# Performance work log

Hardware: AMD Instinct MI355X
Metric: run time of the kernel (lower is better)

The kernel has to match this reference:

```python
import jax, jax.numpy as jnp
import numpy as np
from jax.scipy.special import logsumexp

K = 15          # top-k
N = 4096        # n candidates
BS = 128        # batch size
EPS = 0.1       # entropic regularizer epsilon
MAX_ITER = 200  # Sinkhorn iterations
RANK = 5        # rank of pseudoinverse init
SMALL = 1e-20


def _build_weights():
    """Rank-5 pseudoinverse of Sinkhorn constraint matrix A (as in __init__).
    A maps (f in R^n, g in R^k) -> (f_i + g_c) over rows r = i*(k+1)+c (g_k := 0).
    A^T A = [[(k+1) I_n, J_{n x k}], [J_{k x n}, n I_k]] in closed form."""
    k1 = K + 1
    p = N + K
    G = np.zeros((p, p), dtype=np.float64)
    G[:N, :N] = (k1) * np.eye(N)
    G[:N, N:] = 1.0
    G[N:, :N] = 1.0
    G[N:, N:] = N * np.eye(K)
    w, V = np.linalg.eigh(G)
    idx = np.argsort(w)[-RANK:]
    s = np.sqrt(w[idx])
    V = V[:, idx]                                  # (p, RANK)
    # U = A @ V / s without materializing A (1GB dense):
    vf = V[:N]                                     # (N, RANK)
    vg = np.concatenate([V[N:], np.zeros((1, RANK))], axis=0)  # (k1, RANK)
    U = (vf[:, None, :] + vg[None, :, :]).reshape(N * k1, RANK) / s
    weight1 = (V / s).astype(np.float32)           # (N+K, RANK) = V diag(1/s)
    weight2 = U.T.astype(np.float32)               # (RANK, N*(K+1)) = U^T
    return jnp.asarray(weight1), jnp.asarray(weight2)


def setup_inputs() -> dict:
    key = jax.random.key(0)
    scores = jax.random.normal(key, (BS, N), dtype=jnp.float32)
    tau = jnp.ones((1,), jnp.float32) * 0.1
    weight1, weight2 = _build_weights()
    return {"scores": scores, "tau": tau, "weight1": weight1, "weight2": weight2}


def _sinkhorn(C, mu, nu, Gamma0, weight1, weight2):
    bs, n, k1 = C.shape
    # least-squares warm start for potentials f, g
    b = (C + EPS * jnp.log(Gamma0)).reshape(bs, -1)          # (bs, n*k1)
    x = jnp.einsum('bm,rm->br', b, weight2)                  # (bs, RANK)
    x = jnp.einsum('br,pr->bp', x, weight1)                  # (bs, n+k)
    f = x[:, :n, None]                                       # (bs, n, 1)
    g = jnp.concatenate([x[:, n:], jnp.zeros((bs, 1), C.dtype)], axis=-1)[:, None, :]  # (bs,1,k1)
    elog_mu = EPS * jnp.log(mu)                              # (1, n, 1)
    elog_nu = EPS * jnp.log(nu)                              # (1, 1, k1)

    def step(carry, _):
        f, g = carry
        f = -EPS * logsumexp(-(C - g) / EPS, axis=-1, keepdims=True) + elog_mu
        g = -EPS * logsumexp(-(C - f) / EPS, axis=-2, keepdims=True) + elog_nu
        return (f, g), None

    (f, g), _ = jax.lax.scan(step, (f, g), None, length=MAX_ITER)
    return jnp.exp((-C + f + g) / EPS)


def reference(scores, tau, weight1, weight2):
    bs, n = scores.shape
    k = K
    s = scores[:, :, None]                                   # (bs, n, 1)
    sd = jax.lax.stop_gradient(s)
    max_s = jnp.max(sd)
    min_s = jnp.min(jnp.where(jnp.isneginf(sd), jnp.inf, sd))
    filled = min_s - (max_s - min_s)
    s = jnp.where(jnp.isneginf(s), filled, s)
    anchors = jnp.arange(k, -1, -1, dtype=s.dtype).reshape(1, 1, k + 1)
    C = (s - anchors) ** 2
    C = C / jax.lax.stop_gradient(C.max())
    mu = jnp.full((1, n, 1), 1.0 / n, dtype=s.dtype)
    nu = jnp.concatenate([jnp.full((k,), 1.0 / n), jnp.array([(n - k) / n])]).astype(s.dtype).reshape(1, 1, k + 1)
    # warm-start transport plan Gamma0 from (detached) hard top-k
    topk_val = jax.lax.top_k(jax.lax.stop_gradient(s[..., 0]), k)[0]      # (bs, k)
    Gamma0 = jax.nn.sigmoid(-jnp.abs(topk_val[:, None, :] - s) / tau)     # (bs, n, k)
    Gamma0 = Gamma0 + SMALL
    Gamma0 = Gamma0 / Gamma0.sum(-2, keepdims=True) / n
    Gamma0_last = jnp.clip(1.0 / n - Gamma0.sum(-1, keepdims=True), SMALL, 1.0 - SMALL)
    Gamma0 = jnp.concatenate([Gamma0, Gamma0_last], axis=-1)              # (bs, n, k+1)
    Gamma = _sinkhorn(C, mu, nu, Gamma0, weight1, weight2)
    A = Gamma[:, :, :k] * n
    return A, jnp.linalg.norm(Gamma - Gamma0)
```

## Files before the change

kernel.cpp:

```cpp
#include <hip/hip_runtime.h>
#include <math.h>

#define KK 15
#define K1 16
#define NN 4096
#define BSZ 128
#define NT 512
#define RPT 8
#define NPAIR 4
#define NW 8
#define EPSI 0.1f
#define SMALLC 1e-20f
#define NITER 200
#define W2STRIDE 65536
#define OUT_A_ELEMS (BSZ * NN * KK)
#define TS 20
#define CONV_REL 5e-7f

typedef __attribute__((ext_vector_type(2))) float f2;
typedef __attribute__((ext_vector_type(2))) unsigned u2v;
__device__ __forceinline__ f2 pk_fma(f2 a, f2 b, f2 c){
  return __builtin_elementwise_fma(a, b, c);
}

__device__ __forceinline__ unsigned enc_f32(float f){
  unsigned u = __float_as_uint(f);
  return (u & 0x80000000u) ? ~u : (u | 0x80000000u);
}
__device__ __forceinline__ float dec_f32(unsigned e){
  unsigned u = (e & 0x80000000u) ? (e ^ 0x80000000u) : ~e;
  return __uint_as_float(u);
}


template<int CTRL>
__device__ __forceinline__ float dpp_movf(float x){
  return __uint_as_float((unsigned)__builtin_amdgcn_update_dpp(
      (int)0, (int)__float_as_uint(x), CTRL, 0xF, 0xF, true));
}

__device__ __forceinline__ float xsum16(float r){
#if __has_builtin(__builtin_amdgcn_permlane16_swap)
  u2v s = __builtin_amdgcn_permlane16_swap(__float_as_uint(r), __float_as_uint(r), false, false);
  return __uint_as_float(s.x) + __uint_as_float(s.y);
#else
  return r + __shfl_xor(r, 16);
#endif
}
__device__ __forceinline__ float xsum32(float r){
#if __has_builtin(__builtin_amdgcn_permlane32_swap)
  u2v s = __builtin_amdgcn_permlane32_swap(__float_as_uint(r), __float_as_uint(r), false, false);
  return __uint_as_float(s.x) + __uint_as_float(s.y);
#else
  return r + __shfl_xor(r, 32);
#endif
}

__device__ __forceinline__ int fold_col(int lane){
  int l = lane & 15;
  return ((l & 1) << 3) | ((l & 2) << 1) | ((l & 8) >> 2) | ((l & 4) >> 2);
}

__device__ __forceinline__ float wave_fold16(const float p[K1], int lane){
  float a[8];
  {
    const bool hi = (lane & 1) != 0;
    #pragma unroll
    for (int j = 0; j < 8; ++j){
      float send = hi ? p[j] : p[j + 8];
      float keep = hi ? p[j + 8] : p[j];
      a[j] = keep + dpp_movf<0xB1>(send);
    }
  }
  float bq[4];
  {
    const bool hi = (lane & 2) != 0;
    #pragma unroll
    for (int j = 0; j < 4; ++j){
      float send = hi ? a[j] : a[j + 4];
      float keep = hi ? a[j + 4] : a[j];
      bq[j] = keep + dpp_movf<0x4E>(send);
    }
  }
  float cq[2];
  {
    const bool hi = (lane & 8) != 0;
    float s0 = hi ? bq[0] : bq[2];
    float s1 = hi ? bq[1] : bq[3];
    float k0 = hi ? bq[2] : bq[0];
    float k1 = hi ? bq[3] : bq[1];
    cq[0] = k0 + dpp_movf<0x128>(s0);
    cq[1] = k1 + dpp_movf<0x128>(s1);
  }
  float r;
  {
    const bool hi = (lane & 4) != 0;
    float send = hi ? cq[0] : cq[1];
    float keep = hi ? cq[1] : cq[0];
    r = keep + __shfl_xor(send, 4);
  }
  r = xsum16(r);
  r = xsum32(r);
  return r;
}

__device__ __forceinline__ void block_fold16(const float p[K1], float* wb, float* tb,
                                             int lane, int wv, int tid){
  float r = wave_fold16(p, lane);
  if (lane < 16) wb[wv * K1 + fold_col(lane)] = r;
  __syncthreads();
  if (tid < 16){
    float t = 0.0f;
    #pragma unroll
    for (int q = 0; q < NW; ++q) t += wb[q * K1 + tid];
    tb[tid] = t;
  }
  __syncthreads();
}

__global__ __launch_bounds__(NT, 2) void k_main(
    const float* __restrict__ scores, const float* __restrict__ taup,
    const float* __restrict__ w1, const float* __restrict__ w2,
    float* __restrict__ out, unsigned* __restrict__ ws){
  const int b = blockIdx.x;
  const int tid = threadIdx.x;
  const int lane = tid & 63;
  const int wv = tid >> 6;

  __shared__ float scratch[NN];
  __shared__ float tk[KK];
  __shared__ int tki[KK];
  __shared__ __align__(16) float cbuf[K1];
  __shared__ float wbuf[NW * K1];
  __shared__ __align__(16) float xbuf[K1];
  __shared__ __align__(16) float wbufT[2][K1 * TS];
  __shared__ float rv[NW];
  __shared__ int ri[NW];
  __shared__ float rmn[NW];
  __shared__ unsigned sng[NW];
  __shared__ float statb[4];

  float raw[RPT];
  #pragma unroll
  for (int j = 0; j < RPT; ++j) raw[j] = scores[(size_t)b * NN + tid + NT * j];

  {
    float mx = -INFINITY, mn = INFINITY; unsigned neg = 0u;
    #pragma unroll
    for (int j = 0; j < RPT; ++j){
      float v = raw[j];
      mx = fmaxf(mx, v);
      if (v == -INFINITY) neg = 1u; else mn = fminf(mn, v);
    }
    #pragma unroll
    for (int off = 32; off; off >>= 1){
      mx = fmaxf(mx, __shfl_xor(mx, off));
      mn = fminf(mn, __shfl_xor(mn, off));
      neg |= (unsigned)__shfl_xor((int)neg, off);
    }
    if (lane == 0){ rv[wv] = mx; rmn[wv] = mn; sng[wv] = neg; }
    __syncthreads();
    if (tid == 0){
      for (int q = 1; q < NW; ++q){
        mx = fmaxf(mx, rv[q]); mn = fminf(mn, rmn[q]); neg |= sng[q];
      }
      atomicMax(&ws[0], enc_f32(mx));
      atomicMin(&ws[5], enc_f32(mn));
      if (neg) atomicOr(&ws[1], 1u);
      __threadfence();
      atomicAdd(&ws[3], 1u);
      while (__hip_atomic_load(&ws[3], __ATOMIC_ACQUIRE, __HIP_MEMORY_SCOPE_AGENT) < (unsigned)BSZ)
        __builtin_amdgcn_s_sleep(2);
      statb[0] = dec_f32(__hip_atomic_load(&ws[0], __ATOMIC_RELAXED, __HIP_MEMORY_SCOPE_AGENT));
      statb[1] = dec_f32(__hip_atomic_load(&ws[5], __ATOMIC_RELAXED, __HIP_MEMORY_SCOPE_AGENT));
      statb[2] = __hip_atomic_load(&ws[1], __ATOMIC_RELAXED, __HIP_MEMORY_SCOPE_AGENT) ? 1.0f : 0.0f;
    }
    __syncthreads();
  }

  const float smax = statb[0];
  const float smin_raw = statb[1];
  const bool has_neg = statb[2] != 0.0f;
  const float filled = smin_raw - (smax - smin_raw);
  const float smin_eff = has_neg ? filled : smin_raw;
  const float cmax = fmaxf(fmaxf(smin_eff * smin_eff, smax * smax),
                           fmaxf((smin_eff - 15.0f) * (smin_eff - 15.0f),
                                 (smax - 15.0f) * (smax - 15.0f)));
  const float cinv = 1.0f / cmax;
  const float tauv = taup[0];
  const float invtau = 1.0f / tauv;
  const float inv_n = 1.0f / (float)NN;

  #pragma unroll
  for (int j = 0; j < RPT; ++j){
    float v = raw[j]; if (v == -INFINITY) v = filled;
    scratch[tid + NT * j] = v;
  }
  __syncthreads();

  for (int t = 0; t < KK; ++t){
    float bv = -INFINITY; int bi = NN;
    #pragma unroll
    for (int j = 0; j < RPT; ++j){
      int i = tid + NT * j;
      float v = scratch[i];
      if (v > bv){ bv = v; bi = i; }
    }
    #pragma unroll
    for (int off = 32; off; off >>= 1){
      float ov = __shfl_xor(bv, off);
      int oi = __shfl_xor(bi, off);
      if (ov > bv || (ov == bv && oi < bi)){ bv = ov; bi = oi; }
    }
    if (lane == 0){ rv[wv] = bv; ri[wv] = bi; }
    __syncthreads();
    if (tid == 0){
      for (int q = 1; q < NW; ++q){
        if (rv[q] > bv || (rv[q] == bv && ri[q] < bi)){ bv = rv[q]; bi = ri[q]; }
      }
      tk[t] = bv;
      tki[t] = bi;
      scratch[bi] = -INFINITY;
    }
    __syncthreads();
  }
  if (tid < KK) scratch[tki[tid]] = tk[tid];
  __syncthreads();

  {
    float p[K1];
    float tkr[KK];
    #pragma unroll
    for (int c = 0; c < KK; ++c) tkr[c] = tk[c];
    #pragma unroll
    for (int c = 0; c < K1; ++c) p[c] = 0.0f;
    #pragma unroll
    for (int j = 0; j < RPT; ++j){
      float si = scratch[tid + NT * j];
      #pragma unroll
      for (int c = 0; c < KK; ++c){
        float z = fabsf(tkr[c] - si) * invtau;
        float raw1 = __builtin_amdgcn_rcpf(1.0f + __expf(z)) + SMALLC;
        p[c] += raw1;
      }
    }
    block_fold16(p, wbuf, cbuf, lane, wv, tid);
  }

  float colinv_n[KK];
  {
    float p[K1];
    float tkr[KK];
    #pragma unroll
    for (int c = 0; c < KK; ++c){
      tkr[c] = tk[c];
      colinv_n[c] = (1.0f / cbuf[c]) * inv_n;
    }
    #pragma unroll
    for (int c = 0; c < K1; ++c) p[c] = 0.0f;
    #pragma unroll
    for (int j = 0; j < RPT; ++j){
      int i = tid + NT * j;
      float si = scratch[i];
      float bb[K1];
      float rowpart = 0.0f;
      #pragma unroll
      for (int c = 0; c < KK; ++c){
        float d = si - (float)(KK - c);
        float Cc = d * d * cinv;
        float z = fabsf(tkr[c] - si) * invtau;
        float raw1 = __builtin_amdgcn_rcpf(1.0f + __expf(z)) + SMALLC;
        float g0 = raw1 * colinv_n[c];
        rowpart += g0;
        bb[c] = Cc + EPSI * __logf(g0);
      }
      {
        float Cc = si * si * cinv;
        float g0l = fminf(fmaxf(inv_n - rowpart, SMALLC), 1.0f - SMALLC);
        bb[KK] = Cc + EPSI * __logf(g0l);
      }
      #pragma unroll
      for (int r = 0; r < 5; ++r){
        const float4* wp = (const float4*)(w2 + (size_t)r * W2STRIDE + (size_t)i * K1);
        float4 a0 = wp[0], a1 = wp[1], a2 = wp[2], a3 = wp[3];
        float acc = p[r];
        acc += bb[0] * a0.x + bb[1] * a0.y + bb[2] * a0.z + bb[3] * a0.w;
        acc += bb[4] * a1.x + bb[5] * a1.y + bb[6] * a1.z + bb[7] * a1.w;
        acc += bb[8] * a2.x + bb[9] * a2.y + bb[10] * a2.z + bb[11] * a2.w;
        acc += bb[12] * a3.x + bb[13] * a3.y + bb[14] * a3.z + bb[15] * a3.w;
        p[r] = acc;
      }
    }
    block_fold16(p, wbuf, xbuf, lane, wv, tid);
  }

  float vt[K1];
  {
    float xv[5];
    #pragma unroll
    for (int r = 0; r < 5; ++r) xv[r] = xbuf[r];
    #pragma unroll
    for (int c = 0; c < KK; ++c){
      float g = 0.0f;
      #pragma unroll
      for (int r = 0; r < 5; ++r) g += xv[r] * w1[(size_t)(NN + c) * 5 + r];
      float Bc = expf(-10.0f * cinv * (float)((KK - c) * (KK - c)));
      vt[c] = Bc * expf(g * 10.0f);
    }
    vt[KK] = 1.0f;
  }

  f2 x2[NPAIR];
  #pragma unroll
  for (int q = 0; q < NPAIR; ++q){
    float s0 = scratch[tid + NT * (2 * q)];
    float s1 = scratch[tid + NT * (2 * q + 1)];
    x2[q].x = expf(s0 * (-20.0f * cinv));
    x2[q].y = expf(s1 * (-20.0f * cinv));
  }
  f2 xp[NPAIR][K1];
  #pragma unroll
  for (int q = 0; q < NPAIR; ++q){
    xp[q][0].x = 1.0f; xp[q][0].y = 1.0f;
    xp[q][1] = x2[q];
    #pragma unroll
    for (int c = 2; c < K1; ++c) xp[q][c] = xp[q][c - 1] * x2[q];
  }

  f2 t2[NPAIR];
  const float nmul = ((lane & 15) < KK) ? 1.0f : 4081.0f;
  float pv2 = 0.0f, pv1 = 0.0f;
  int pcnt = -1;
  #pragma unroll 1
  for (int it = 0; it < NITER; ++it){
    const int ph = it & 1;
    #pragma unroll
    for (int q = 0; q < NPAIR; ++q){
      f2 h; h.x = vt[KK]; h.y = vt[KK];
      #pragma unroll
      for (int c = KK - 1; c >= 0; --c){
        f2 vc; vc.x = vt[c]; vc.y = vt[c];
        h = pk_fma(h, x2[q], vc);
      }
      t2[q].x = __builtin_amdgcn_rcpf(h.x);
      t2[q].y = __builtin_amdgcn_rcpf(h.y);
    }
    float p[K1];
    #pragma unroll
    for (int c = 0; c < K1; ++c){
      f2 s = t2[0] * xp[0][c];
      #pragma unroll
      for (int q = 1; q < NPAIR; ++q) s = pk_fma(t2[q], xp[q][c], s);
      p[c] = s.x + s.y;
    }
    float r = wave_fold16(p, lane);
    if (lane < 16) wbufT[ph][fold_col(lane) * TS + wv] = r;
    __syncthreads();
    float md = -1.0f;
    float wout = 0.0f;
    if (lane < 16){
      const float* wp = &wbufT[ph][lane * TS];
      float4 a4 = *(const float4*)wp;
      float4 b4 = *(const float4*)(wp + 4);
      float t = ((a4.x + a4.y) + (a4.z + a4.w)) + ((b4.x + b4.y) + (b4.z + b4.w));
      float wnew = nmul * __builtin_amdgcn_rcpf(t);
      md = fabsf(wnew - pv1) - CONV_REL * pv1;
      wout = wnew;
      if (pcnt >= 1){
        float d1 = pv1 - pv2;
        float d2 = wnew - pv1;
        float den = d2 - d1;
        float acc = wnew - d2 * d2 * __builtin_amdgcn_rcpf(den);
        bool ok = (fabsf(d2) < fabsf(d1)) &&
                  (acc > 0.1f * wnew) && (acc < 10.0f * wnew) &&
                  (fabsf(d2) > 4.0f * CONV_REL * wnew);
        if (ok){ wout = acc; pcnt = -1; }
      }
      pcnt++;
      pv2 = pv1; pv1 = wout;
    }
    int conv = __all(md <= 0.0f);
    #pragma unroll
    for (int c = 0; c < K1; ++c)
      vt[c] = __uint_as_float((unsigned)__builtin_amdgcn_readlane(
                  (int)__float_as_uint(wout), c));
    if (conv) break;
  }

  float nrm = 0.0f;
  {
    float tkr[KK];
    #pragma unroll
    for (int c = 0; c < KK; ++c) tkr[c] = tk[c];
    #pragma unroll
    for (int q = 0; q < NPAIR; ++q){
      #pragma unroll
      for (int half = 0; half < 2; ++half){
        int i = tid + NT * (2 * q + half);
        float si = scratch[i];
        float tin = (half ? t2[q].y : t2[q].x) * inv_n;
        float rowpart = 0.0f;
        float gamv[KK];
        float gaml;
        #pragma unroll
        for (int c = 0; c < KK; ++c){
          float xc = half ? xp[q][c].y : xp[q][c].x;
          float gam = (tin * xc) * vt[c];
          float z = fabsf(tkr[c] - si) * invtau;
          float raw1 = __builtin_amdgcn_rcpf(1.0f + __expf(z)) + SMALLC;
          float g0 = raw1 * colinv_n[c];
          rowpart += g0;
          float d = gam - g0;
          nrm += d * d;
          gamv[c] = gam * (float)NN;
        }
        {
          float xc = half ? xp[q][KK].y : xp[q][KK].x;
          gaml = (tin * xc) * vt[KK];
          float g0l = fminf(fmaxf(inv_n - rowpart, SMALLC), 1.0f - SMALLC);
          float d = gaml - g0l;
          nrm += d * d;
        }
        float* op = out + (size_t)(b * NN + i) * KK;
        #pragma unroll
        for (int c = 0; c < KK; ++c) op[c] = gamv[c];
      }
    }
  }
  #pragma unroll
  for (int off = 32; off; off >>= 1) nrm += __shfl_xor(nrm, off);
  if (lane == 0) rv[wv] = nrm;
  __syncthreads();
  if (tid == 0){
    float t = 0.0f;
    for (int q = 0; q < NW; ++q) t += rv[q];
    atomicAdd(reinterpret_cast<float*>(ws) + 2, t);
    __threadfence();
    unsigned prev = atomicAdd(&ws[4], 1u);
    if (prev == (unsigned)(BSZ - 1)){
      float n2 = __hip_atomic_load(reinterpret_cast<float*>(ws) + 2,
                                   __ATOMIC_RELAXED, __HIP_MEMORY_SCOPE_AGENT);
      out[OUT_A_ELEMS] = sqrtf(n2);
    }
  }
}

extern "C" void kernel_launch(void* const* d_in, const int* in_sizes, int n_in,
                              void* d_out, int out_size, void* d_ws, size_t ws_size,
                              hipStream_t stream){
  const float* scores = (const float*)d_in[0];
  const float* tau    = (const float*)d_in[1];
  const float* w1     = (const float*)d_in[2];
  const float* w2     = (const float*)d_in[3];
  float* out = (float*)d_out;
  unsigned* ws = (unsigned*)d_ws;

  hipMemsetAsync(ws, 0x00, 20, stream);
  hipMemsetAsync((char*)ws + 20, 0xFF, 4, stream);

  k_main<<<BSZ, NT, 0, stream>>>(scores, tau, w1, w2, out, ws);
}
```

Measured before the change: 154.9 us.

## Use vector-wide Aitken extrapolation for column scalings and parallelize top-k merge

Replaces the per-column Aitken delta-squared acceleration of the Sinkhorn column potentials with a single vector extrapolation. The shared step factor is computed from DPP cross-lane sums of the relative increments, and all 16 columns are extrapolated together only when every column stays in bounds. The goal is to cut the number of Sinkhorn iterations before the convergence test passes. It also swaps the serial thread-0 merge of per-wave top-k candidates for a shuffle reduction over 8 lanes. The new extrapolation rule changes numerical behaviour and could converge more slowly or to a slightly different result.

```diff
diff --git a/kernel.cpp b/kernel.cpp
--- a/kernel.cpp
+++ b/kernel.cpp
@@ -39,6 +39,11 @@
       (int)0, (int)__float_as_uint(x), CTRL, 0xF, 0xF, true));
 }
 
+__device__ __forceinline__ float bcast_lane0(float x){
+  return __uint_as_float((unsigned)__builtin_amdgcn_readlane(
+      (int)__float_as_uint(x), 0));
+}
+
 __device__ __forceinline__ float xsum16(float r){
 #if __has_builtin(__builtin_amdgcn_permlane16_swap)
   u2v s = __builtin_amdgcn_permlane16_swap(__float_as_uint(r), __float_as_uint(r), false, false);
@@ -54,6 +59,14 @@
 #else
   return r + __shfl_xor(r, 32);
 #endif
+}
+
+__device__ __forceinline__ float sum16_all(float v){
+  v += dpp_movf<0x128>(v);
+  v += dpp_movf<0x124>(v);
+  v += dpp_movf<0x4E>(v);
+  v += dpp_movf<0xB1>(v);
+  return v;
 }
 
 __device__ __forceinline__ int fold_col(int lane){
@@ -214,13 +227,19 @@
     }
     if (lane == 0){ rv[wv] = bv; ri[wv] = bi; }
     __syncthreads();
-    if (tid == 0){
-      for (int q = 1; q < NW; ++q){
-        if (rv[q] > bv || (rv[q] == bv && ri[q] < bi)){ bv = rv[q]; bi = ri[q]; }
-      }
-      tk[t] = bv;
-      tki[t] = bi;
-      scratch[bi] = -INFINITY;
+    {
+      float mv = -INFINITY; int mi = NN;
+      if (tid < NW){ mv = rv[tid]; mi = ri[tid]; }
+      #pragma unroll
+      for (int off = 4; off; off >>= 1){
+        float ov = __shfl_xor(mv, off);
+        int oi = __shfl_xor(mi, off);
+        if (ov > mv || (ov == mv && oi < mi)){ mv = ov; mi = oi; }
+      }
+      if (tid == 0){
+        tk[t] = mv; tki[t] = mi;
+        scratch[mi] = -INFINITY;
+      }
     }
     __syncthreads();
   }
@@ -366,19 +385,30 @@
       float wnew = nmul * __builtin_amdgcn_rcpf(t);
       md = fabsf(wnew - pv1) - CONV_REL * pv1;
       wout = wnew;
-      if (pcnt >= 1){
-        float d1 = pv1 - pv2;
-        float d2 = wnew - pv1;
-        float den = d2 - d1;
-        float acc = wnew - d2 * d2 * __builtin_amdgcn_rcpf(den);
-        bool ok = (fabsf(d2) < fabsf(d1)) &&
-                  (acc > 0.1f * wnew) && (acc < 10.0f * wnew) &&
-                  (fabsf(d2) > 4.0f * CONV_REL * wnew);
-        if (ok){ wout = acc; pcnt = -1; }
-      }
-      pcnt++;
-      pv2 = pv1; pv1 = wout;
-    }
+    }
+    if (pcnt >= 1){
+      float r1 = 0.0f, r2 = 0.0f;
+      if (lane < 16){
+        float winv = __builtin_amdgcn_rcpf(wout);
+        r1 = (pv1 - pv2) * winv;
+        r2 = (wout - pv1) * winv;
+      }
+      float s12 = sum16_all(r1 * r2);
+      float s11 = sum16_all(r1 * r1);
+      float s12b = bcast_lane0(s12);
+      float s11b = bcast_lane0(s11);
+      int anymove = __any((lane < 16) && (fabsf(r2) > 4.0f * CONV_REL));
+      float fac = s12b * __builtin_amdgcn_rcpf(s11b - s12b);
+      float acc = wout * (1.0f + r2 * fac);
+      int okbr = (lane < 16) ? (acc > 0.1f * wout && acc < 10.0f * wout) : 1;
+      int allbr = __all(okbr);
+      if ((s12b > 0.0f) && (s12b < 0.97f * s11b) && anymove && allbr){
+        if (lane < 16) wout = acc;
+        pcnt = -1;
+      }
+    }
+    pcnt++;
+    pv2 = pv1; pv1 = wout;
     int conv = __all(md <= 0.0f);
     #pragma unroll
     for (int c = 0; c < K1; ++c)
```

After: 150.5 us. 2.8% less time.
